# Optimization experiments

Hardware: AMD Instinct MI355X
Metric: run time of the kernel (lower is better)

Reference implementation:

```python
import jax, jax.numpy as jnp
import numpy as np

B, G, T, N = 2, 4, 64, 300
D = 256          # detr_dim == feature_dim
R = 4            # ffn_dim_ratio
MD = 32          # motion_dim


def _xavier(key, shape):
    lim = (6.0 / (shape[0] + shape[1])) ** 0.5
    return jax.random.uniform(key, shape, jnp.float32, -lim, lim)


def setup_inputs() -> dict:
    key = jax.random.key(0)
    ks = jax.random.split(key, 16)
    feats = jax.random.normal(ks[0], (B, G, T, N, D), jnp.float32)
    boxes = jax.random.uniform(ks[1], (B, G, T, N, 4), jnp.float32)
    masks = jax.random.bernoulli(ks[2], 0.3, (B, G, T, N))
    # per-trajectory permutation of frame ids 0..T-1 (unique -> unambiguous scatter)
    u = jax.random.uniform(ks[3], (B, G, N, T))
    times = jnp.swapaxes(jnp.argsort(u, axis=-1).astype(jnp.int32), 2, 3)  # [B,G,T,N]
    return {
        'trajectory_features': feats,
        'trajectory_boxes': boxes,
        'trajectory_masks': masks,
        'trajectory_times': times,
        'adp_w1': _xavier(ks[4], (D, D * R)), 'adp_b1': jnp.zeros((D * R,), jnp.float32),
        'adp_w2': _xavier(ks[5], (D * R, D)), 'adp_b2': jnp.zeros((D,), jnp.float32),
        'norm_g': jnp.ones((D,), jnp.float32), 'norm_b': jnp.zeros((D,), jnp.float32),
        'mot_w1': _xavier(ks[6], (12, MD // 2)), 'mot_b1': jnp.zeros((MD // 2,), jnp.float32),
        'mot_w2': _xavier(ks[7], (MD // 2, MD)), 'mot_b2': jnp.zeros((MD,), jnp.float32),
        'fus_w1': _xavier(ks[8], (D + MD, D)), 'fus_b1': jnp.zeros((D,), jnp.float32),
        'fus_w2': _xavier(ks[9], (D, D)), 'fus_b2': jnp.zeros((D,), jnp.float32),
        'ffn_w1': _xavier(ks[10], (D, D * R)), 'ffn_b1': jnp.zeros((D * R,), jnp.float32),
        'ffn_w2': _xavier(ks[11], (D * R, D)), 'ffn_b2': jnp.zeros((D,), jnp.float32),
        'fnorm_g': jnp.ones((D,), jnp.float32), 'fnorm_b': jnp.zeros((D,), jnp.float32),
    }


def _ffn(x, w1, b1, w2, b2):
    return jax.nn.gelu(x @ w1 + b1, approximate=False) @ w2 + b2


def _ln(x, g, b):
    m = x.mean(-1, keepdims=True)
    v = ((x - m) ** 2).mean(-1, keepdims=True)
    return (x - m) / jnp.sqrt(v + 1e-5) * g + b


def _motion_features(boxes, masks, times, mot_w1, mot_b1, mot_w2, mot_b2):
    # boxes [B,G,T,N,4] -> trajectory-major [B,G,N,T,*]
    b_, g_, t_, n_ = masks.shape
    md = mot_b2.shape[0]
    bx = jnp.swapaxes(boxes, 2, 3)              # [B,G,N,T,4]
    valid = ~jnp.swapaxes(masks, 2, 3)          # [B,G,N,T]
    tm = jnp.swapaxes(times, 2, 3)              # [B,G,N,T]
    # sort valid entries first, by time (stable)
    order = jnp.argsort(jnp.where(valid, tm, t_ + 1), axis=-1)
    sb = jnp.take_along_axis(bx, order[..., None], axis=3)   # sorted boxes
    st = jnp.take_along_axis(tm, order, axis=-1)             # sorted times
    cnt = valid.sum(-1)                                      # [B,G,N]
    pos = jnp.arange(t_)
    in_count = pos[None, None, None, :] < cnt[..., None]
    dt = jnp.maximum(st - jnp.roll(st, 1, axis=-1), 1).astype(sb.dtype)[..., None]
    mask_v = ((pos >= 1)[None, None, None, :] & in_count)[..., None]
    vel = jnp.where(mask_v, (sb - jnp.roll(sb, 1, axis=3)) / dt, 0.0)
    mask_a = ((pos >= 2)[None, None, None, :] & in_count)[..., None]
    acc = jnp.where(mask_a, (vel - jnp.roll(vel, 1, axis=3)) / dt, 0.0)
    mv = jnp.concatenate([sb, vel, acc], axis=-1)            # [B,G,N,T,12]
    enc = jax.nn.gelu(mv @ mot_w1 + mot_b1, approximate=False) @ mot_w2 + mot_b2
    write = in_count & (cnt >= 2)[..., None] & (st < t_)
    frame = jnp.where(write, st, t_)                         # t_ -> dropped
    bi, gi, ni, ti = jnp.meshgrid(jnp.arange(b_), jnp.arange(g_), jnp.arange(n_),
                                  jnp.arange(t_), indexing='ij')
    out = jnp.zeros((b_, g_, t_, n_, md), sb.dtype)
    return out.at[bi, gi, frame, ni].set(enc, mode='drop')


def reference(trajectory_features, trajectory_boxes, trajectory_masks, trajectory_times,
              adp_w1, adp_b1, adp_w2, adp_b2, norm_g, norm_b,
              mot_w1, mot_b1, mot_w2, mot_b2,
              fus_w1, fus_b1, fus_w2, fus_b2,
              ffn_w1, ffn_b1, ffn_w2, ffn_b2, fnorm_g, fnorm_b):
    x = trajectory_features + _ffn(trajectory_features, adp_w1, adp_b1, adp_w2, adp_b2)
    x = _ln(x, norm_g, norm_b)
    motion = _motion_features(trajectory_boxes, trajectory_masks, trajectory_times,
                              mot_w1, mot_b1, mot_w2, mot_b2)
    cat = jnp.concatenate([x, motion], axis=-1)
    fused = jax.nn.gelu(cat @ fus_w1 + fus_b1, approximate=False) @ fus_w2 + fus_b2
    fused = fused + _ffn(fused, ffn_w1, ffn_b1, ffn_w2, ffn_b2)
    fused = _ln(fused, fnorm_g, fnorm_b)
    return fused, motion
```

## Files before the change

### kernel.cpp

```cpp
#include <hip/hip_runtime.h>

typedef __bf16 bf16x8 __attribute__((ext_vector_type(8)));
typedef float f32x4 __attribute__((ext_vector_type(4)));

namespace {

constexpr int T_ = 64;
constexpr int N_ = 300;
constexpr int MD_ = 32;
constexpr int BG_ = 8;
constexpr long MROWS_ = (long)BG_ * T_ * N_;
constexpr long FUSED_N = MROWS_ * 256;
constexpr int MB = 128;

constexpr long PA1 = 0;
constexpr long PA2 = 262144;
constexpr long PF1 = 524288;
constexpr long PF2 = 598016;
constexpr long PN1 = 663552;
constexpr long PN2 = 925696;

__device__ __forceinline__ float gelu_f(float x) {
  const float x2 = x * x;
  const float z2 = x * fmaf(x2, 0.07135481627f, 1.5957691216f);
  const float t = __builtin_amdgcn_rcpf(1.0f + __expf(z2));
  return x * (1.0f - t);
}

__device__ __forceinline__ float gelu_exact(float x) {
  return 0.5f * x * (1.0f + erff(x * 0.7071067811865476f));
}

__global__ void k_zero_flag(int* f) { *f = 0; }

__global__ void k_detect_mask(const unsigned char* __restrict__ m, int nbytes,
                              int* __restrict__ f) {
  int i = blockIdx.x * 256 + threadIdx.x;
  if (i < nbytes && (i & 3) != 0 && m[i] != 0) atomicOr(f, 1);
}

__global__ __launch_bounds__(256)
void k_motion(const float* __restrict__ boxes, const void* __restrict__ masks,
              const int* __restrict__ times,
              const float* __restrict__ mw1, const float* __restrict__ mb1,
              const float* __restrict__ mw2, const float* __restrict__ mb2,
              float* __restrict__ motion, const int* __restrict__ flagp) {
  __shared__ int slot[4][T_];
  __shared__ int sts[4][T_];
  __shared__ float sbx[4][T_][4];
  __shared__ float otile[4][T_][MD_];
  const int tid = threadIdx.x;
  const int w = tid >> 6, l = tid & 63;
  const int traj = blockIdx.x * 4 + w;
  const int bg = traj / N_, n = traj - bg * N_;
  const int isbool = *flagp;
  const long idx = ((long)bg * T_ + l) * N_ + n;
  const bool msk = isbool ? (((const unsigned char*)masks)[idx] != 0)
                          : (((const int*)masks)[idx] != 0);
  const bool valid = !msk;
  const int tm = times[idx];

  slot[w][l] = -1;
  sts[w][l] = 0;
  *(float4*)&sbx[w][l][0] = make_float4(0.f, 0.f, 0.f, 0.f);
  __syncthreads();
  if (valid) slot[w][tm] = l;
  __syncthreads();

  const int ot = slot[w][l];
  const bool vp = ot >= 0;
  const unsigned long long bal = __ballot(vp);
  const int cnt = __builtin_popcountll(bal);
  const int pos = __builtin_popcountll(bal & ((1ull << l) - 1ull));
  if (vp) {
    sts[w][pos] = l;
    const float4 bx = *(const float4*)(boxes + (((long)bg * T_ + ot) * N_ + n) * 4);
    *(float4*)&sbx[w][pos][0] = bx;
  }
  __syncthreads();

  const int stp = sts[w][l];
  const int stm1 = sts[w][(l + 63) & 63];
  const float4 sb = *(const float4*)&sbx[w][l][0];
  const float4 sbm = *(const float4*)&sbx[w][(l + 63) & 63][0];
  const float dt = (float)max(stp - stm1, 1);
  const float inv = 1.0f / dt;
  const bool okv = (l >= 1) && (l < cnt);
  float v0 = okv ? (sb.x - sbm.x) * inv : 0.f;
  float v1 = okv ? (sb.y - sbm.y) * inv : 0.f;
  float v2 = okv ? (sb.z - sbm.z) * inv : 0.f;
  float v3 = okv ? (sb.w - sbm.w) * inv : 0.f;
  const float p0 = __shfl_up(v0, 1, 64);
  const float p1 = __shfl_up(v1, 1, 64);
  const float p2 = __shfl_up(v2, 1, 64);
  const float p3 = __shfl_up(v3, 1, 64);
  const bool oka = (l >= 2) && (l < cnt);
  const float a0 = oka ? (v0 - p0) * inv : 0.f;
  const float a1 = oka ? (v1 - p1) * inv : 0.f;
  const float a2 = oka ? (v2 - p2) * inv : 0.f;
  const float a3 = oka ? (v3 - p3) * inv : 0.f;

  const float mv[12] = {sb.x, sb.y, sb.z, sb.w, v0, v1, v2, v3, a0, a1, a2, a3};
  float e1[16];
#pragma unroll
  for (int i = 0; i < 16; ++i) {
    float a = mb1[i];
#pragma unroll
    for (int c = 0; c < 12; ++c) a = fmaf(mv[c], mw1[c * 16 + i], a);
    e1[i] = gelu_exact(a);
  }
  float enc[32];
#pragma unroll
  for (int o = 0; o < 32; ++o) {
    float a = mb2[o];
#pragma unroll
    for (int i = 0; i < 16; ++i) a = fmaf(e1[i], mw2[i * 32 + o], a);
    enc[o] = a;
  }

#pragma unroll
  for (int c = 0; c < 32; c += 4)
    *(float4*)&otile[w][l][c] = make_float4(0.f, 0.f, 0.f, 0.f);
  __syncthreads();
  if (l < cnt && cnt >= 2) {
#pragma unroll
    for (int c = 0; c < 32; ++c) otile[w][stp][c] = enc[c];
  }
  __syncthreads();

  float* mbase = motion + ((long)bg * T_ * N_ + n) * MD_;
  const float4* srcv = (const float4*)&otile[w][l][0];
  float4* dstv = (float4*)(mbase + (long)l * N_ * MD_);
#pragma unroll
  for (int q = 0; q < 8; ++q) dstv[q] = srcv[q];
}

__global__ void k_pack(const float* __restrict__ W, __bf16* __restrict__ P,
                       int K, int NN) {
  int gid = blockIdx.x * 256 + threadIdx.x;
  int total = (K >> 5) * (NN >> 4) * 64;
  if (gid >= total) return;
  int l = gid & 63, f = gid >> 6;
  int NT = NN >> 4;
  int kb = f / NT, nt = f - kb * NT;
  int krow = kb * 32 + (l >> 4) * 8;
  int col = nt * 16 + (l & 15);
  bf16x8 v;
#pragma unroll
  for (int e = 0; e < 8; ++e) v[e] = (__bf16)W[(long)(krow + e) * NN + col];
  *(bf16x8*)(P + (long)gid * 8) = v;
}

template <int KBN, int JN, int RSH>
__device__ __forceinline__ void mm_l2(const char* reg, const __bf16* bb,
                                      const long kstride, const int row0,
                                      const int lr, const int lk,
                                      f32x4 (&acc)[4][JN]) {
  bf16x8 bA[JN], bB[JN];
#pragma unroll
  for (int j = 0; j < JN; ++j) bA[j] = *(const bf16x8*)(bb + ((long)j << 9));
  if (KBN > 1) {
#pragma unroll
    for (int j = 0; j < JN; ++j)
      bB[j] = *(const bf16x8*)(bb + kstride + ((long)j << 9));
  }
#pragma unroll
  for (int kb = 0; kb < KBN; ++kb) {
    bf16x8 a[4];
#pragma unroll
    for (int m = 0; m < 4; ++m) {
      const int row = row0 + m * 16 + lr;
      a[m] = *(const bf16x8*)(reg + ((long)row << RSH) +
                              ((((kb << 2) + lk) ^ (row & 7)) << 4));
    }
    __builtin_amdgcn_s_setprio(1);
#pragma unroll
    for (int j = 0; j < JN; ++j) {
      const bf16x8 b = (kb & 1) ? bB[j] : bA[j];
#pragma unroll
      for (int m = 0; m < 4; ++m)
        acc[m][j] =
            __builtin_amdgcn_mfma_f32_16x16x32_bf16(a[m], b, acc[m][j], 0, 0, 0);
    }
    __builtin_amdgcn_s_setprio(0);
    if (kb < KBN - 2) {
#pragma unroll
      for (int j = 0; j < JN; ++j) {
        const bf16x8 v =
            *(const bf16x8*)(bb + (long)(kb + 2) * kstride + ((long)j << 9));
        if (kb & 1) bB[j] = v; else bA[j] = v;
      }
    }
  }
}

__global__ __launch_bounds__(512, 1)
void k_mfma(const float* __restrict__ feats, const float* __restrict__ motion,
            const __bf16* __restrict__ pw,
            const float* __restrict__ ba1, const float* __restrict__ ba2,
            const float* __restrict__ ng, const float* __restrict__ nb,
            const float* __restrict__ bf1, const float* __restrict__ bf2,
            const float* __restrict__ bn1, const float* __restrict__ bn2,
            const float* __restrict__ fg, const float* __restrict__ fb,
            float* __restrict__ out) {
  __shared__ __align__(16) char smem[106496];
  __shared__ float red[MB][4][2];
  char* regA = smem;
  char* regB = smem + 65536;
  char* regM = smem + 98304;

  const int tid = threadIdx.x;
  const int l = tid & 63, wid = tid >> 6;
  const int lr = l & 15, lk = l >> 4;
  const int wr = wid >> 2;
  const int wn = wid & 3;
  const int colb = wn * 64;
  const int row0 = wr * 64;
  const long rowbase = (long)blockIdx.x * MB;

  const __bf16* pa1 = pw + PA1;
  const __bf16* pa2 = pw + PA2;
  const __bf16* pf1 = pw + PF1;
  const __bf16* pf2 = pw + PF2;
  const __bf16* pn1 = pw + PN1;
  const __bf16* pn2 = pw + PN2;

  auto ldb = [&](const __bf16* pb, int frag) -> bf16x8 {
    return *(const bf16x8*)(pb + ((long)frag << 9) + (l << 3));
  };
  auto store_gelu128 = [&](char* reg, const f32x4 (&acc)[4][2]) {
#pragma unroll
    for (int j = 0; j < 2; ++j) {
      const int col = wn * 32 + j * 16 + lr;
#pragma unroll
      for (int m = 0; m < 4; ++m)
#pragma unroll
        for (int e = 0; e < 4; ++e) {
          const int row = row0 + m * 16 + lk * 4 + e;
          *(__bf16*)(reg + row * 256 + (((col >> 3) ^ (row & 7)) << 4) +
                     ((col & 7) << 1)) = (__bf16)gelu_f(acc[m][j][e]);
        }
    }
  };
  auto ln_stats = [&](const f32x4 (&acc)[4][4], float (&mean)[4][4],
                      float (&rstd)[4][4]) {
    float s1[4][4], s2[4][4];
#pragma unroll
    for (int m = 0; m < 4; ++m)
#pragma unroll
      for (int e = 0; e < 4; ++e) { s1[m][e] = 0.f; s2[m][e] = 0.f; }
#pragma unroll
    for (int m = 0; m < 4; ++m)
#pragma unroll
      for (int j = 0; j < 4; ++j)
#pragma unroll
        for (int e = 0; e < 4; ++e) {
          s1[m][e] += acc[m][j][e];
          s2[m][e] += acc[m][j][e] * acc[m][j][e];
        }
#pragma unroll
    for (int o = 1; o < 16; o <<= 1)
#pragma unroll
      for (int m = 0; m < 4; ++m)
#pragma unroll
        for (int e = 0; e < 4; ++e) {
          s1[m][e] += __shfl_xor(s1[m][e], o);
          s2[m][e] += __shfl_xor(s2[m][e], o);
        }
    if (lr == 0) {
#pragma unroll
      for (int m = 0; m < 4; ++m)
#pragma unroll
        for (int e = 0; e < 4; ++e) {
          const int row = row0 + m * 16 + lk * 4 + e;
          red[row][wn][0] = s1[m][e];
          red[row][wn][1] = s2[m][e];
        }
    }
    __syncthreads();
#pragma unroll
    for (int m = 0; m < 4; ++m)
#pragma unroll
      for (int e = 0; e < 4; ++e) {
        const int row = row0 + m * 16 + lk * 4 + e;
        const float S1 =
            red[row][0][0] + red[row][1][0] + red[row][2][0] + red[row][3][0];
        const float S2 =
            red[row][0][1] + red[row][1][1] + red[row][2][1] + red[row][3][1];
        const float mu = S1 * (1.0f / 256.0f);
        const float var = S2 * (1.0f / 256.0f) - mu * mu;
        mean[m][e] = mu;
        rstd[m][e] = rsqrtf(var + 1e-5f);
      }
  };

  f32x4 acc2[4][4];
#pragma unroll
  for (int j = 0; j < 4; ++j) {
    const int col = colb + j * 16 + lr;
    const float bv = ba2[col];
#pragma unroll
    for (int m = 0; m < 4; ++m)
#pragma unroll
      for (int e = 0; e < 4; ++e) {
        const int row = row0 + m * 16 + lk * 4 + e;
        acc2[m][j][e] = bv + feats[(rowbase + row) * 256 + col];
      }
  }
#pragma unroll
  for (int it = 0; it < 8; ++it) {
    const int c = tid + it * 512;
    const int row = c >> 5, cc = c & 31;
    const float* src = feats + (rowbase + row) * 256 + cc * 8;
    bf16x8 v;
#pragma unroll
    for (int e = 0; e < 8; ++e) v[e] = (__bf16)src[e];
    *(bf16x8*)(regA + row * 512 + ((cc ^ (row & 7)) << 4)) = v;
  }
  __syncthreads();

#pragma unroll 1
  for (int ch = 0; ch < 8; ++ch) {
    f32x4 acc1[4][2];
#pragma unroll
    for (int j = 0; j < 2; ++j) {
      const float bv = ba1[ch * 128 + wn * 32 + j * 16 + lr];
#pragma unroll
      for (int m = 0; m < 4; ++m) acc1[m][j] = {bv, bv, bv, bv};
    }
    mm_l2<8, 2, 9>(regA, pa1 + ((long)(ch * 8 + wn * 2) << 9) + (l << 3),
                   (long)64 << 9, row0, lr, lk, acc1);
    __syncthreads();
    store_gelu128(regB, acc1);
    __syncthreads();
    mm_l2<4, 4, 8>(regB, pa2 + ((long)(ch * 64 + wn * 4) << 9) + (l << 3),
                   (long)16 << 9, row0, lr, lk, acc2);
  }

  {
    float mean[4][4], rstd[4][4];
    ln_stats(acc2, mean, rstd);
#pragma unroll
    for (int j = 0; j < 4; ++j) {
      const int col = colb + j * 16 + lr;
      const float gv = ng[col], bv = nb[col];
#pragma unroll
      for (int m = 0; m < 4; ++m)
#pragma unroll
        for (int e = 0; e < 4; ++e) {
          const int row = row0 + m * 16 + lk * 4 + e;
          const float v = (acc2[m][j][e] - mean[m][e]) * rstd[m][e] * gv + bv;
          *(__bf16*)(regA + row * 512 + (((col >> 3) ^ (row & 7)) << 4) +
                     ((col & 7) << 1)) = (__bf16)v;
        }
    }
    {
      const int row = tid >> 2, cc = tid & 3;
      const float* src = motion + (rowbase + row) * 32 + cc * 8;
      bf16x8 v;
#pragma unroll
      for (int e = 0; e < 8; ++e) v[e] = (__bf16)src[e];
      *(bf16x8*)(regM + row * 64 + ((cc ^ (row & 3)) << 4)) = v;
    }
  }
  __syncthreads();

  {
    f32x4 accD[4][4];
#pragma unroll
    for (int j = 0; j < 4; ++j) {
      const float bv = bf2[colb + j * 16 + lr];
#pragma unroll
      for (int m = 0; m < 4; ++m) accD[m][j] = {bv, bv, bv, bv};
    }
#pragma unroll 1
    for (int n0 = 0; n0 < 2; ++n0) {
      f32x4 accB[4][2];
#pragma unroll
      for (int j = 0; j < 2; ++j) {
        const float bv = bf1[n0 * 128 + wn * 32 + j * 16 + lr];
#pragma unroll
        for (int m = 0; m < 4; ++m) accB[m][j] = {bv, bv, bv, bv};
      }
      mm_l2<8, 2, 9>(regA, pf1 + ((long)(n0 * 8 + wn * 2) << 9) + (l << 3),
                     (long)16 << 9, row0, lr, lk, accB);
      {
        bf16x8 a[4];
#pragma unroll
        for (int m = 0; m < 4; ++m) {
          const int row = row0 + m * 16 + lr;
          a[m] = *(const bf16x8*)(regM + row * 64 + ((lk ^ (row & 3)) << 4));
        }
#pragma unroll
        for (int j = 0; j < 2; ++j) {
          const bf16x8 b = ldb(pf1, 128 + n0 * 8 + wn * 2 + j);
#pragma unroll
          for (int m = 0; m < 4; ++m)
            accB[m][j] = __builtin_amdgcn_mfma_f32_16x16x32_bf16(
                a[m], b, accB[m][j], 0, 0, 0);
        }
      }
      __syncthreads();
      store_gelu128(regB, accB);
      __syncthreads();
      mm_l2<4, 4, 8>(regB, pf2 + ((long)(n0 * 64 + wn * 4) << 9) + (l << 3),
                     (long)16 << 9, row0, lr, lk, accD);
    }
#pragma unroll
    for (int j = 0; j < 4; ++j) {
      const int col = colb + j * 16 + lr;
      const float bv = bn2[col];
#pragma unroll
      for (int m = 0; m < 4; ++m)
#pragma unroll
        for (int e = 0; e < 4; ++e) {
          const int row = row0 + m * 16 + lk * 4 + e;
          const float fv = accD[m][j][e];
          *(__bf16*)(regA + row * 512 + (((col >> 3) ^ (row & 7)) << 4) +
                     ((col & 7) << 1)) = (__bf16)fv;
          acc2[m][j][e] = fv + bv;
        }
    }
  }
  __syncthreads();

#pragma unroll 1
  for (int ch = 0; ch < 8; ++ch) {
    f32x4 acc1[4][2];
#pragma unroll
    for (int j = 0; j < 2; ++j) {
      const float bv = bn1[ch * 128 + wn * 32 + j * 16 + lr];
#pragma unroll
      for (int m = 0; m < 4; ++m) acc1[m][j] = {bv, bv, bv, bv};
    }
    mm_l2<8, 2, 9>(regA, pn1 + ((long)(ch * 8 + wn * 2) << 9) + (l << 3),
                   (long)64 << 9, row0, lr, lk, acc1);
    __syncthreads();
    store_gelu128(regB, acc1);
    __syncthreads();
    mm_l2<4, 4, 8>(regB, pn2 + ((long)(ch * 64 + wn * 4) << 9) + (l << 3),
                   (long)16 << 9, row0, lr, lk, acc2);
  }

  {
    float mean[4][4], rstd[4][4];
    ln_stats(acc2, mean, rstd);
#pragma unroll
    for (int j = 0; j < 4; ++j) {
      const int col = colb + j * 16 + lr;
      const float gv = fg[col], bv = fb[col];
#pragma unroll
      for (int m = 0; m < 4; ++m)
#pragma unroll
        for (int e = 0; e < 4; ++e) {
          const int row = row0 + m * 16 + lk * 4 + e;
          out[(rowbase + row) * 256 + col] =
              (acc2[m][j][e] - mean[m][e]) * rstd[m][e] * gv + bv;
        }
    }
  }
}

}

extern "C" void kernel_launch(void* const* d_in, const int* in_sizes, int n_in,
                              void* d_out, int out_size, void* d_ws, size_t ws_size,
                              hipStream_t stream) {
  const float* feats = (const float*)d_in[0];
  const float* boxes = (const float*)d_in[1];
  const void*  masks = d_in[2];
  const int*   times = (const int*)d_in[3];
  const float* wa1 = (const float*)d_in[4];
  const float* ba1 = (const float*)d_in[5];
  const float* wa2 = (const float*)d_in[6];
  const float* ba2 = (const float*)d_in[7];
  const float* ng  = (const float*)d_in[8];
  const float* nb  = (const float*)d_in[9];
  const float* mw1 = (const float*)d_in[10];
  const float* mb1 = (const float*)d_in[11];
  const float* mw2 = (const float*)d_in[12];
  const float* mb2 = (const float*)d_in[13];
  const float* wf1 = (const float*)d_in[14];
  const float* bf1 = (const float*)d_in[15];
  const float* wf2 = (const float*)d_in[16];
  const float* bf2 = (const float*)d_in[17];
  const float* wn1 = (const float*)d_in[18];
  const float* bn1 = (const float*)d_in[19];
  const float* wn2 = (const float*)d_in[20];
  const float* bn2 = (const float*)d_in[21];
  const float* fg  = (const float*)d_in[22];
  const float* fb  = (const float*)d_in[23];

  float* out_fused = (float*)d_out;
  float* out_motion = out_fused + FUSED_N;
  int* flag = (int*)d_ws;
  __bf16* pw = (__bf16*)((char*)d_ws + 256);

  const int mask_elems = in_sizes[2];

  k_zero_flag<<<1, 1, 0, stream>>>(flag);
  k_detect_mask<<<(mask_elems + 255) / 256, 256, 0, stream>>>(
      (const unsigned char*)masks, mask_elems, flag);
  k_motion<<<(BG_ * N_) / 4, 256, 0, stream>>>(boxes, masks, times, mw1, mb1, mw2,
                                               mb2, out_motion, flag);

  auto packn = [&](const float* W, long off, int K, int NN) {
    const int total = (K / 32) * (NN / 16) * 64;
    k_pack<<<(total + 255) / 256, 256, 0, stream>>>(W, pw + off, K, NN);
  };
  packn(wa1, PA1, 256, 1024);
  packn(wa2, PA2, 1024, 256);
  packn(wf1, PF1, 288, 256);
  packn(wf2, PF2, 256, 256);
  packn(wn1, PN1, 256, 1024);
  packn(wn2, PN2, 1024, 256);

  k_mfma<<<(int)(MROWS_ / MB), 512, 0, stream>>>(
      feats, out_motion, pw, ba1, ba2, ng, nb, bf1, bf2, bn1, bn2, fg, fb,
      out_fused);
}
```

Measured before the change: 636.1 us.

## Restructure FFN hidden-chunk loops into produce/consume with transposed MFMA and register-resident fragments

The two 256->1024->256 FFN loops now process 256-wide hidden chunks in 4 rounds instead of 128-wide chunks in 8. In the produce step each wave computes the hidden tile transposed (weight fragment as the A operand, activations as B), with prefetched weight fragments. GELU outputs are rearranged with cross-lane shuffles into fragment-ordered bf16 vectors stored directly to LDS, which replaces the scattered per-element swizzled stores. The consume step reads those fragments contiguously and uses MFMA priority hints. This halves the number of barriers per FFN and enlarges the hidden staging buffer into the freed shared memory, at the cost of extra shuffle work and higher register pressure.

```diff
diff --git a/kernel.cpp b/kernel.cpp
--- a/kernel.cpp
+++ b/kernel.cpp
@@ -203,11 +203,12 @@
             const float* __restrict__ bn1, const float* __restrict__ bn2,
             const float* __restrict__ fg, const float* __restrict__ fb,
             float* __restrict__ out) {
-  __shared__ __align__(16) char smem[106496];
-  __shared__ float red[MB][4][2];
+  __shared__ __align__(16) char smem[131072];
   char* regA = smem;
+  char* hbuf = smem + 65536;
   char* regB = smem + 65536;
   char* regM = smem + 98304;
+  float* redp = (float*)(smem + 106496);
 
   const int tid = threadIdx.x;
   const int l = tid & 63, wid = tid >> 6;
@@ -217,6 +218,9 @@
   const int colb = wn * 64;
   const int row0 = wr * 64;
   const long rowbase = (long)blockIdx.x * MB;
+  const bool lsel = l < 32;
+  const int slo = lr + ((l & 16) ? 32 : 0);
+  const int shi = slo + 16;
 
   const __bf16* pa1 = pw + PA1;
   const __bf16* pa2 = pw + PA2;
@@ -228,6 +232,90 @@
   auto ldb = [&](const __bf16* pb, int frag) -> bf16x8 {
     return *(const bf16x8*)(pb + ((long)frag << 9) + (l << 3));
   };
+  auto lda8 = [&](int kb, int xrt) -> bf16x8 {
+    const int row = xrt * 16 + lr;
+    return *(const bf16x8*)(regA + row * 512 +
+                            ((((kb << 2) + lk) ^ (row & 7)) << 4));
+  };
+
+  auto produce = [&](const __bf16* pb1, const float* b1, int r) {
+    const int nt0 = (r * 8 + wid) * 2;
+    f32x4 t0[8], t1[8];
+    {
+      const float4 bA = *(const float4*)(b1 + nt0 * 16 + lk * 4);
+      const float4 bB = *(const float4*)(b1 + nt0 * 16 + 16 + lk * 4);
+#pragma unroll
+      for (int x = 0; x < 8; ++x) {
+        t0[x] = f32x4{bA.x, bA.y, bA.z, bA.w};
+        t1[x] = f32x4{bB.x, bB.y, bB.z, bB.w};
+      }
+    }
+    bf16x8 wfA = ldb(pb1, nt0), wfB = ldb(pb1, nt0 + 1);
+#pragma unroll
+    for (int kbs = 0; kbs < 8; ++kbs) {
+      bf16x8 nA, nB;
+      if (kbs < 7) {
+        nA = ldb(pb1, (kbs + 1) * 64 + nt0);
+        nB = ldb(pb1, (kbs + 1) * 64 + nt0 + 1);
+      }
+      __builtin_amdgcn_s_setprio(1);
+#pragma unroll
+      for (int x = 0; x < 8; ++x) {
+        const bf16x8 xf = lda8(kbs, x);
+        t0[x] = __builtin_amdgcn_mfma_f32_16x16x32_bf16(wfA, xf, t0[x], 0, 0, 0);
+        t1[x] = __builtin_amdgcn_mfma_f32_16x16x32_bf16(wfB, xf, t1[x], 0, 0, 0);
+      }
+      __builtin_amdgcn_s_setprio(0);
+      wfA = nA; wfB = nB;
+    }
+#pragma unroll
+    for (int x = 0; x < 8; ++x) {
+      float TA[4], TB[4];
+#pragma unroll
+      for (int rr = 0; rr < 4; ++rr) {
+        TA[rr] = gelu_f(t0[x][rr]);
+        TB[rr] = gelu_f(t1[x][rr]);
+      }
+      bf16x8 hf;
+#pragma unroll
+      for (int rr = 0; rr < 4; ++rr) {
+        const float a0 = __shfl(TA[rr], slo, 64);
+        const float b0 = __shfl(TB[rr], slo, 64);
+        const float a1 = __shfl(TA[rr], shi, 64);
+        const float b1v = __shfl(TB[rr], shi, 64);
+        hf[rr] = (__bf16)(lsel ? a0 : b0);
+        hf[4 + rr] = (__bf16)(lsel ? a1 : b1v);
+      }
+      *(bf16x8*)(hbuf + (((wid * 8 + x) * 64 + l) << 4)) = hf;
+    }
+  };
+  auto consume = [&](const __bf16* pb2, int r, f32x4 (&acc)[4][4]) {
+    bf16x8 bw0[4], bw1[4];
+#pragma unroll
+    for (int j = 0; j < 4; ++j) bw0[j] = ldb(pb2, (r * 8) * 16 + wn * 4 + j);
+#pragma unroll
+    for (int kbl = 0; kbl < 8; ++kbl) {
+      if (kbl < 7) {
+#pragma unroll
+        for (int j = 0; j < 4; ++j)
+          bw1[j] = ldb(pb2, (r * 8 + kbl + 1) * 16 + wn * 4 + j);
+      }
+      bf16x8 a[4];
+#pragma unroll
+      for (int m = 0; m < 4; ++m)
+        a[m] = *(const bf16x8*)(hbuf + (((kbl * 8 + wr * 4 + m) * 64 + l) << 4));
+      __builtin_amdgcn_s_setprio(1);
+#pragma unroll
+      for (int j = 0; j < 4; ++j)
+#pragma unroll
+        for (int m = 0; m < 4; ++m)
+          acc[m][j] = __builtin_amdgcn_mfma_f32_16x16x32_bf16(a[m], bw0[j],
+                                                              acc[m][j], 0, 0, 0);
+      __builtin_amdgcn_s_setprio(0);
+#pragma unroll
+      for (int j = 0; j < 4; ++j) bw0[j] = bw1[j];
+    }
+  };
   auto store_gelu128 = [&](char* reg, const f32x4 (&acc)[4][2]) {
 #pragma unroll
     for (int j = 0; j < 2; ++j) {
@@ -273,8 +361,8 @@
 #pragma unroll
         for (int e = 0; e < 4; ++e) {
           const int row = row0 + m * 16 + lk * 4 + e;
-          red[row][wn][0] = s1[m][e];
-          red[row][wn][1] = s2[m][e];
+          redp[(row * 4 + wn) * 2 + 0] = s1[m][e];
+          redp[(row * 4 + wn) * 2 + 1] = s2[m][e];
         }
     }
     __syncthreads();
@@ -283,10 +371,10 @@
 #pragma unroll
       for (int e = 0; e < 4; ++e) {
         const int row = row0 + m * 16 + lk * 4 + e;
-        const float S1 =
-            red[row][0][0] + red[row][1][0] + red[row][2][0] + red[row][3][0];
-        const float S2 =
-            red[row][0][1] + red[row][1][1] + red[row][2][1] + red[row][3][1];
+        const float S1 = redp[(row * 4 + 0) * 2] + redp[(row * 4 + 1) * 2] +
+                         redp[(row * 4 + 2) * 2] + redp[(row * 4 + 3) * 2];
+        const float S2 = redp[(row * 4 + 0) * 2 + 1] + redp[(row * 4 + 1) * 2 + 1] +
+                         redp[(row * 4 + 2) * 2 + 1] + redp[(row * 4 + 3) * 2 + 1];
         const float mu = S1 * (1.0f / 256.0f);
         const float var = S2 * (1.0f / 256.0f) - mu * mu;
         mean[m][e] = mu;
@@ -320,21 +408,11 @@
   __syncthreads();
 
 #pragma unroll 1
-  for (int ch = 0; ch < 8; ++ch) {
-    f32x4 acc1[4][2];
-#pragma unroll
-    for (int j = 0; j < 2; ++j) {
-      const float bv = ba1[ch * 128 + wn * 32 + j * 16 + lr];
-#pragma unroll
-      for (int m = 0; m < 4; ++m) acc1[m][j] = {bv, bv, bv, bv};
-    }
-    mm_l2<8, 2, 9>(regA, pa1 + ((long)(ch * 8 + wn * 2) << 9) + (l << 3),
-                   (long)64 << 9, row0, lr, lk, acc1);
+  for (int r = 0; r < 4; ++r) {
+    produce(pa1, ba1, r);
     __syncthreads();
-    store_gelu128(regB, acc1);
+    consume(pa2, r, acc2);
     __syncthreads();
-    mm_l2<4, 4, 8>(regB, pa2 + ((long)(ch * 64 + wn * 4) << 9) + (l << 3),
-                   (long)16 << 9, row0, lr, lk, acc2);
   }
 
   {
@@ -425,21 +503,11 @@
   __syncthreads();
 
 #pragma unroll 1
-  for (int ch = 0; ch < 8; ++ch) {
-    f32x4 acc1[4][2];
-#pragma unroll
-    for (int j = 0; j < 2; ++j) {
-      const float bv = bn1[ch * 128 + wn * 32 + j * 16 + lr];
-#pragma unroll
-      for (int m = 0; m < 4; ++m) acc1[m][j] = {bv, bv, bv, bv};
-    }
-    mm_l2<8, 2, 9>(regA, pn1 + ((long)(ch * 8 + wn * 2) << 9) + (l << 3),
-                   (long)64 << 9, row0, lr, lk, acc1);
+  for (int r = 0; r < 4; ++r) {
+    produce(pn1, bn1, r);
     __syncthreads();
-    store_gelu128(regB, acc1);
+    consume(pn2, r, acc2);
     __syncthreads();
-    mm_l2<4, 4, 8>(regB, pn2 + ((long)(ch * 64 + wn * 4) << 9) + (l << 3),
-                   (long)16 << 9, row0, lr, lk, acc2);
   }
 
   {
```

After: 669.9 us. +5.3%, slower.
